# Performance work log

Measured on AMD Instinct MI355X. Metric: run time of the kernel, lower is better.

The kernel has to match this reference:

```python
import jax, jax.numpy as jnp
import numpy as np

ALPHA = 1.0  # Student-t degrees of freedom (module default)


def setup_inputs() -> dict:
    key = jax.random.key(0)
    k1, k2 = jax.random.split(key)
    N, D, K = 65536, 512, 256
    x = jax.random.normal(k1, (N, D), dtype=jnp.float32)
    clusters = jax.random.normal(k2, (K, D), dtype=jnp.float32)
    return {"x": x, "clusters": clusters}


def reference(x, clusters):
    # Squared Euclidean distance via norm expansion + GEMM (same math as
    # sum((x[:,None,:] - clusters[None,:,:])**2, axis=2); original then takes
    # sqrt and immediately re-squares, so we use sqdist directly).
    x_sq = jnp.sum(x * x, axis=1, keepdims=True)            # [N,1]
    c_sq = jnp.sum(clusters * clusters, axis=1)             # [K]
    sqdist = x_sq + c_sq[None, :] - 2.0 * (x @ clusters.T)  # [N,K]
    sqdist = jnp.maximum(sqdist, 0.0)
    # Student's t kernel: q_ij = (1 + d^2/alpha)^(-(alpha+1)/2)
    q = (1.0 + sqdist / ALPHA) ** (-(ALPHA + 1.0) / 2.0)
    # Row-normalize to soft assignments
    return q / jnp.sum(q, axis=1, keepdims=True)
```

## Files before the change

### kernel.cpp

```cpp
#include <hip/hip_runtime.h>
#include <hip/hip_bf16.h>
#include <stdint.h>

typedef unsigned short u16;
typedef __attribute__((ext_vector_type(8))) short short8_t;
typedef __attribute__((ext_vector_type(4))) float f32x4;

#define D_DIM 512
#define K_CL  256
#define BM    128

__device__ __forceinline__ u16 f2bf(float f) {
  union { float f; uint32_t u; } v; v.f = f;
  uint32_t r = v.u + 0x7fffu + ((v.u >> 16) & 1u);
  return (u16)(r >> 16);
}

__global__ void prep_kernel(const float* __restrict__ clusters,
                            u16* __restrict__ cb, float* __restrict__ csq) {
  int k = blockIdx.x;
  int t = threadIdx.x;
  float4 f = ((const float4*)(clusters + (size_t)k * D_DIM))[t];
  ushort4 u;
  u.x = f2bf(f.x); u.y = f2bf(f.y); u.z = f2bf(f.z); u.w = f2bf(f.w);
  ((ushort4*)(cb + (size_t)k * D_DIM))[t] = u;
  float s = f.x*f.x + f.y*f.y + f.z*f.z + f.w*f.w;
  #pragma unroll
  for (int m = 1; m < 64; m <<= 1) s += __shfl_xor(s, m, 64);
  __shared__ float part[2];
  if ((t & 63) == 0) part[t >> 6] = s;
  __syncthreads();
  if (t == 0) csq[k] = part[0] + part[1];
}

__global__ __launch_bounds__(512)
void cluster_kernel(const float* __restrict__ x,
                    const u16* __restrict__ cb,
                    const float* __restrict__ csq,
                    float* __restrict__ out) {
  __shared__ u16  lA[BM * 32];
  __shared__ u16  lB[K_CL * 32];
  __shared__ float xsq_lds[BM];
  __shared__ float csq_lds[K_CL];
  __shared__ float rowsum[4 * BM];

  const int tid   = threadIdx.x;
  const int lane  = tid & 63;
  const int w     = tid >> 6;
  const int quad  = lane >> 4;
  const int l16   = lane & 15;
  const int wave_m = w >> 2;
  const int wave_n = w & 3;
  const int row0  = blockIdx.x * BM;

  if (tid < K_CL) csq_lds[tid] = csq[tid];

  const int ar = tid >> 2;
  const int ac = (tid & 3) * 8;
  const float* xg = x + (size_t)(row0 + ar) * D_DIM + ac;
  short8_t* aw = (short8_t*)&lA[ar * 32 + ac];

  const int aro = (wave_m * 64 + l16) * 32 + quad * 8;
  const int bro = (wave_n * 64 + l16) * 32 + quad * 8;

  f32x4 acc[4][4];
  #pragma unroll
  for (int i = 0; i < 4; ++i)
    #pragma unroll
    for (int j = 0; j < 4; ++j)
      acc[i][j] = (f32x4){0.f, 0.f, 0.f, 0.f};

  float sq = 0.f;
  const int boff0 = tid * 16;

  for (int kk = 0; kk < D_DIM; kk += 32) {
    if (kk) __syncthreads();
    float4 f0 = *(const float4*)(xg + kk);
    float4 f1 = *(const float4*)(xg + kk + 4);
    sq += f0.x*f0.x + f0.y*f0.y + f0.z*f0.z + f0.w*f0.w
        + f1.x*f1.x + f1.y*f1.y + f1.z*f1.z + f1.w*f1.w;
    union { u16 u[8]; short8_t v; } pk;
    pk.u[0]=f2bf(f0.x); pk.u[1]=f2bf(f0.y); pk.u[2]=f2bf(f0.z); pk.u[3]=f2bf(f0.w);
    pk.u[4]=f2bf(f1.x); pk.u[5]=f2bf(f1.y); pk.u[6]=f2bf(f1.z); pk.u[7]=f2bf(f1.w);
    *aw = pk.v;
    #pragma unroll
    for (int i = 0; i < 2; ++i) {
      int off = boff0 + i * 8192;
      int n = off >> 6;
      int inrow = off & 63;
      const u16* src = cb + (size_t)n * D_DIM + kk + (inrow >> 1);
      __builtin_amdgcn_global_load_lds(
          (const __attribute__((address_space(1))) void*)src,
          (__attribute__((address_space(3))) void*)((char*)lB + off),
          16, 0, 0);
    }
    __syncthreads();
    short8_t aF[4], bF[4];
    #pragma unroll
    for (int mi = 0; mi < 4; ++mi)
      aF[mi] = *(const short8_t*)&lA[aro + mi * 16 * 32];
    #pragma unroll
    for (int ni = 0; ni < 4; ++ni)
      bF[ni] = *(const short8_t*)&lB[bro + ni * 16 * 32];
    #pragma unroll
    for (int mi = 0; mi < 4; ++mi)
      #pragma unroll
      for (int ni = 0; ni < 4; ++ni)
        acc[mi][ni] = __builtin_amdgcn_mfma_f32_16x16x32_bf16(
            aF[mi], bF[ni], acc[mi][ni], 0, 0, 0);
  }

  sq += __shfl_xor(sq, 1, 64);
  sq += __shfl_xor(sq, 2, 64);
  if ((tid & 3) == 0) xsq_lds[ar] = sq;
  __syncthreads();

  #pragma unroll
  for (int mi = 0; mi < 4; ++mi) {
    #pragma unroll
    for (int v = 0; v < 4; ++v) {
      int row = wave_m * 64 + mi * 16 + quad * 4 + v;
      float xs = xsq_lds[row];
      float s = 0.f;
      #pragma unroll
      for (int ni = 0; ni < 4; ++ni) {
        int col = wave_n * 64 + ni * 16 + l16;
        float d = xs + csq_lds[col] - 2.0f * acc[mi][ni][v];
        d = fmaxf(d, 0.f);
        float q = 1.0f / (1.0f + d);
        acc[mi][ni][v] = q;
        s += q;
      }
      s += __shfl_xor(s, 1, 64);
      s += __shfl_xor(s, 2, 64);
      s += __shfl_xor(s, 4, 64);
      s += __shfl_xor(s, 8, 64);
      if (l16 == 0) rowsum[wave_n * BM + row] = s;
    }
  }
  __syncthreads();

  #pragma unroll
  for (int mi = 0; mi < 4; ++mi) {
    #pragma unroll
    for (int v = 0; v < 4; ++v) {
      int row = wave_m * 64 + mi * 16 + quad * 4 + v;
      float tot = rowsum[row] + rowsum[BM + row] + rowsum[2*BM + row] + rowsum[3*BM + row];
      float inv = 1.0f / tot;
      float* orow = out + (size_t)(row0 + row) * K_CL;
      #pragma unroll
      for (int ni = 0; ni < 4; ++ni) {
        int col = wave_n * 64 + ni * 16 + l16;
        orow[col] = acc[mi][ni][v] * inv;
      }
    }
  }
}

extern "C" void kernel_launch(void* const* d_in, const int* in_sizes, int n_in,
                              void* d_out, int out_size, void* d_ws, size_t ws_size,
                              hipStream_t stream) {
  const float* x        = (const float*)d_in[0];
  const float* clusters = (const float*)d_in[1];
  float* out = (float*)d_out;
  const int N = in_sizes[0] / D_DIM;

  u16*   cb  = (u16*)d_ws;
  float* csq = (float*)((char*)d_ws + (size_t)K_CL * D_DIM * sizeof(u16));

  prep_kernel<<<K_CL, 128, 0, stream>>>(clusters, cb, csq);
  cluster_kernel<<<N / BM, 512, 0, stream>>>(x, cb, csq, out);
}
```

Before: 218.4 us.

## Double-buffer swizzled cluster tiles and load x directly into MFMA fragments

Restructures the GEMM main loop. Each wave now owns 16 rows by all 256 clusters, and x is loaded straight from global memory into registers as MFMA A fragments, skipping the LDS staging of A. Cluster tiles use BK=64 with an XOR-swizzled, double-buffered LDS layout, so the next tile's load overlaps the current MFMAs and only one barrier is needed per step. The row-sum reduction stays within each wave, removing the LDS and barrier epilogue, and the division becomes a fast rcp. Costs are more accumulator registers per thread, less reuse of B across waves, and an approximate reciprocal.

```diff
diff --git a/kernel.cpp b/kernel.cpp
--- a/kernel.cpp
+++ b/kernel.cpp
@@ -1,5 +1,4 @@
 #include <hip/hip_runtime.h>
-#include <hip/hip_bf16.h>
 #include <stdint.h>
 
 typedef unsigned short u16;
@@ -9,11 +8,22 @@
 #define D_DIM 512
 #define K_CL  256
 #define BM    128
+#define BK    64
+#define NSTEP (D_DIM / BK)
 
 __device__ __forceinline__ u16 f2bf(float f) {
   union { float f; uint32_t u; } v; v.f = f;
   uint32_t r = v.u + 0x7fffu + ((v.u >> 16) & 1u);
   return (u16)(r >> 16);
+}
+
+__device__ __forceinline__ short8_t pack8(float4 f0, float4 f1) {
+  union { u16 u[8]; short8_t v; } pk;
+  pk.u[0] = f2bf(f0.x); pk.u[1] = f2bf(f0.y);
+  pk.u[2] = f2bf(f0.z); pk.u[3] = f2bf(f0.w);
+  pk.u[4] = f2bf(f1.x); pk.u[5] = f2bf(f1.y);
+  pk.u[6] = f2bf(f1.z); pk.u[7] = f2bf(f1.w);
+  return pk.v;
 }
 
 __global__ void prep_kernel(const float* __restrict__ clusters,
@@ -33,127 +43,131 @@
   if (t == 0) csq[k] = part[0] + part[1];
 }
 
-__global__ __launch_bounds__(512)
+__global__ __launch_bounds__(512, 4)
 void cluster_kernel(const float* __restrict__ x,
                     const u16* __restrict__ cb,
                     const float* __restrict__ csq,
                     float* __restrict__ out) {
-  __shared__ u16  lA[BM * 32];
-  __shared__ u16  lB[K_CL * 32];
-  __shared__ float xsq_lds[BM];
-  __shared__ float csq_lds[K_CL];
-  __shared__ float rowsum[4 * BM];
+  __shared__ u16 lB[2 * K_CL * BK];
 
-  const int tid   = threadIdx.x;
-  const int lane  = tid & 63;
-  const int w     = tid >> 6;
-  const int quad  = lane >> 4;
-  const int l16   = lane & 15;
-  const int wave_m = w >> 2;
-  const int wave_n = w & 3;
-  const int row0  = blockIdx.x * BM;
+  const int tid  = threadIdx.x;
+  const int lane = tid & 63;
+  const int w    = tid >> 6;
+  const int l16  = lane & 15;
+  const int quad = lane >> 4;
+  const int row0 = blockIdx.x * BM;
 
-  if (tid < K_CL) csq_lds[tid] = csq[tid];
+  const int arow = row0 + w * 16 + l16;
+  const float4* xg = (const float4*)(x + (size_t)arow * D_DIM + quad * 8);
 
-  const int ar = tid >> 2;
-  const int ac = (tid & 3) * 8;
-  const float* xg = x + (size_t)(row0 + ar) * D_DIM + ac;
-  short8_t* aw = (short8_t*)&lA[ar * 32 + ac];
+  const int o0   = tid * 16;
+  const int n0   = o0 >> 7;
+  const int skb0 = (o0 & 127) ^ ((n0 & 7) << 4);
+  const int o1   = 8192 + tid * 16;
+  const int n1   = o1 >> 7;
+  const int skb1 = (o1 & 127) ^ ((n1 & 7) << 4);
+  const u16* sp0 = cb + (size_t)n0 * D_DIM + (skb0 >> 1);
+  const u16* sp1 = cb + (size_t)n1 * D_DIM + (skb1 >> 1);
 
-  const int aro = (wave_m * 64 + l16) * 32 + quad * 8;
-  const int bro = (wave_n * 64 + l16) * 32 + quad * 8;
+  const int c3 = (l16 & 3) << 4;
+  const int h  = (l16 & 4) << 4;
+  const int p  = l16 * 128 + ((quad * 16) ^ c3);
+  const int p0 = p + h;
+  const int p1 = p + (h ^ 64);
 
-  f32x4 acc[4][4];
+  f32x4 acc[16];
   #pragma unroll
-  for (int i = 0; i < 4; ++i)
-    #pragma unroll
-    for (int j = 0; j < 4; ++j)
-      acc[i][j] = (f32x4){0.f, 0.f, 0.f, 0.f};
+  for (int i = 0; i < 16; ++i) acc[i] = (f32x4){0.f, 0.f, 0.f, 0.f};
+
+  {
+    char* dstb = (char*)lB + tid * 16;
+    __builtin_amdgcn_global_load_lds((const __attribute__((address_space(1))) void*)sp0,
+        (__attribute__((address_space(3))) void*)(dstb),          16, 0, 0);
+    __builtin_amdgcn_global_load_lds((const __attribute__((address_space(1))) void*)sp1,
+        (__attribute__((address_space(3))) void*)(dstb + 8192),   16, 0, 0);
+    __builtin_amdgcn_global_load_lds((const __attribute__((address_space(1))) void*)(sp0 + 65536),
+        (__attribute__((address_space(3))) void*)(dstb + 16384),  16, 0, 0);
+    __builtin_amdgcn_global_load_lds((const __attribute__((address_space(1))) void*)(sp1 + 65536),
+        (__attribute__((address_space(3))) void*)(dstb + 24576),  16, 0, 0);
+  }
+  float4 a0 = xg[0], a1 = xg[1], a2 = xg[8], a3 = xg[9];
 
   float sq = 0.f;
-  const int boff0 = tid * 16;
 
-  for (int kk = 0; kk < D_DIM; kk += 32) {
-    if (kk) __syncthreads();
-    float4 f0 = *(const float4*)(xg + kk);
-    float4 f1 = *(const float4*)(xg + kk + 4);
-    sq += f0.x*f0.x + f0.y*f0.y + f0.z*f0.z + f0.w*f0.w
-        + f1.x*f1.x + f1.y*f1.y + f1.z*f1.z + f1.w*f1.w;
-    union { u16 u[8]; short8_t v; } pk;
-    pk.u[0]=f2bf(f0.x); pk.u[1]=f2bf(f0.y); pk.u[2]=f2bf(f0.z); pk.u[3]=f2bf(f0.w);
-    pk.u[4]=f2bf(f1.x); pk.u[5]=f2bf(f1.y); pk.u[6]=f2bf(f1.z); pk.u[7]=f2bf(f1.w);
-    *aw = pk.v;
+  for (int step = 0; step < NSTEP; ++step) {
+    __syncthreads();
+
+    sq += a0.x*a0.x + a0.y*a0.y + a0.z*a0.z + a0.w*a0.w
+        + a1.x*a1.x + a1.y*a1.y + a1.z*a1.z + a1.w*a1.w
+        + a2.x*a2.x + a2.y*a2.y + a2.z*a2.z + a2.w*a2.w
+        + a3.x*a3.x + a3.y*a3.y + a3.z*a3.z + a3.w*a3.w;
+    short8_t aF0 = pack8(a0, a1);
+    short8_t aF1 = pack8(a2, a3);
+
+    if (step + 1 < NSTEP) {
+      xg += 16;
+      a0 = xg[0]; a1 = xg[1]; a2 = xg[8]; a3 = xg[9];
+      sp0 += BK; sp1 += BK;
+      char* dstb = (char*)lB + (((step + 1) & 1) << 15) + tid * 16;
+      __builtin_amdgcn_global_load_lds((const __attribute__((address_space(1))) void*)sp0,
+          (__attribute__((address_space(3))) void*)(dstb),          16, 0, 0);
+      __builtin_amdgcn_global_load_lds((const __attribute__((address_space(1))) void*)sp1,
+          (__attribute__((address_space(3))) void*)(dstb + 8192),   16, 0, 0);
+      __builtin_amdgcn_global_load_lds((const __attribute__((address_space(1))) void*)(sp0 + 65536),
+          (__attribute__((address_space(3))) void*)(dstb + 16384),  16, 0, 0);
+      __builtin_amdgcn_global_load_lds((const __attribute__((address_space(1))) void*)(sp1 + 65536),
+          (__attribute__((address_space(3))) void*)(dstb + 24576),  16, 0, 0);
+    }
+
+    const char* pb = (const char*)lB + ((step & 1) << 15);
+    const short8_t* q0 = (const short8_t*)(pb + p0);
+    const short8_t* q1 = (const short8_t*)(pb + p1);
     #pragma unroll
-    for (int i = 0; i < 2; ++i) {
-      int off = boff0 + i * 8192;
-      int n = off >> 6;
-      int inrow = off & 63;
-      const u16* src = cb + (size_t)n * D_DIM + kk + (inrow >> 1);
-      __builtin_amdgcn_global_load_lds(
-          (const __attribute__((address_space(1))) void*)src,
-          (__attribute__((address_space(3))) void*)((char*)lB + off),
-          16, 0, 0);
+    for (int ni = 0; ni < 16; ++ni) {
+      short8_t b0 = q0[ni * 128];
+      short8_t b1 = q1[ni * 128];
+      acc[ni] = __builtin_amdgcn_mfma_f32_16x16x32_bf16(aF0, b0, acc[ni], 0, 0, 0);
+      acc[ni] = __builtin_amdgcn_mfma_f32_16x16x32_bf16(aF1, b1, acc[ni], 0, 0, 0);
     }
-    __syncthreads();
-    short8_t aF[4], bF[4];
-    #pragma unroll
-    for (int mi = 0; mi < 4; ++mi)
-      aF[mi] = *(const short8_t*)&lA[aro + mi * 16 * 32];
-    #pragma unroll
-    for (int ni = 0; ni < 4; ++ni)
-      bF[ni] = *(const short8_t*)&lB[bro + ni * 16 * 32];
-    #pragma unroll
-    for (int mi = 0; mi < 4; ++mi)
-      #pragma unroll
-      for (int ni = 0; ni < 4; ++ni)
-        acc[mi][ni] = __builtin_amdgcn_mfma_f32_16x16x32_bf16(
-            aF[mi], bF[ni], acc[mi][ni], 0, 0, 0);
   }
 
-  sq += __shfl_xor(sq, 1, 64);
-  sq += __shfl_xor(sq, 2, 64);
-  if ((tid & 3) == 0) xsq_lds[ar] = sq;
-  __syncthreads();
+  sq += __shfl_xor(sq, 16, 64);
+  sq += __shfl_xor(sq, 32, 64);
+  float xs[4];
+  #pragma unroll
+  for (int v = 0; v < 4; ++v)
+    xs[v] = __shfl(sq, quad * 4 + v, 64);
 
+  float cs[16];
   #pragma unroll
-  for (int mi = 0; mi < 4; ++mi) {
+  for (int ni = 0; ni < 16; ++ni) cs[ni] = csq[ni * 16 + l16];
+
+  float rs[4] = {0.f, 0.f, 0.f, 0.f};
+  #pragma unroll
+  for (int ni = 0; ni < 16; ++ni) {
     #pragma unroll
     for (int v = 0; v < 4; ++v) {
-      int row = wave_m * 64 + mi * 16 + quad * 4 + v;
-      float xs = xsq_lds[row];
-      float s = 0.f;
-      #pragma unroll
-      for (int ni = 0; ni < 4; ++ni) {
-        int col = wave_n * 64 + ni * 16 + l16;
-        float d = xs + csq_lds[col] - 2.0f * acc[mi][ni][v];
-        d = fmaxf(d, 0.f);
-        float q = 1.0f / (1.0f + d);
-        acc[mi][ni][v] = q;
-        s += q;
-      }
-      s += __shfl_xor(s, 1, 64);
-      s += __shfl_xor(s, 2, 64);
-      s += __shfl_xor(s, 4, 64);
-      s += __shfl_xor(s, 8, 64);
-      if (l16 == 0) rowsum[wave_n * BM + row] = s;
+      float d = xs[v] + cs[ni] - 2.0f * acc[ni][v];
+      d = fmaxf(d, 0.f);
+      float qv = __builtin_amdgcn_rcpf(1.0f + d);
+      acc[ni][v] = qv;
+      rs[v] += qv;
     }
   }
-  __syncthreads();
-
   #pragma unroll
-  for (int mi = 0; mi < 4; ++mi) {
+  for (int v = 0; v < 4; ++v) {
+    rs[v] += __shfl_xor(rs[v], 1, 64);
+    rs[v] += __shfl_xor(rs[v], 2, 64);
+    rs[v] += __shfl_xor(rs[v], 4, 64);
+    rs[v] += __shfl_xor(rs[v], 8, 64);
+    rs[v] = __builtin_amdgcn_rcpf(rs[v]);
+  }
+  #pragma unroll
+  for (int v = 0; v < 4; ++v) {
+    float* orow = out + (size_t)(row0 + w * 16 + quad * 4 + v) * K_CL;
     #pragma unroll
-    for (int v = 0; v < 4; ++v) {
-      int row = wave_m * 64 + mi * 16 + quad * 4 + v;
-      float tot = rowsum[row] + rowsum[BM + row] + rowsum[2*BM + row] + rowsum[3*BM + row];
-      float inv = 1.0f / tot;
-      float* orow = out + (size_t)(row0 + row) * K_CL;
-      #pragma unroll
-      for (int ni = 0; ni < 4; ++ni) {
-        int col = wave_n * 64 + ni * 16 + l16;
-        orow[col] = acc[mi][ni][v] * inv;
-      }
-    }
+    for (int ni = 0; ni < 16; ++ni)
+      orow[ni * 16 + l16] = acc[ni][v] * rs[v];
   }
 }
 
```

After: 219.4 us. About the same (+0.5%).
